# Kernel optimization log

Measured on AMD Instinct MI355X. Metric: run time of the kernel, lower is better.

## Reference

```python
import jax, jax.numpy as jnp
import numpy as np

ALPHA = 0.5  # mixing weight between dot-product and wedge-norm terms


def setup_inputs() -> dict:
    key = jax.random.key(0)
    kq, kk, kv = jax.random.split(key, 3)
    B, L, H, E = 2, 2048, 8, 32
    queries = jax.random.normal(kq, (B, L, H, E), dtype=jnp.float32)
    keys = jax.random.normal(kk, (B, L, H, E), dtype=jnp.float32)
    values = jax.random.normal(kv, (B, L, H, E), dtype=jnp.float32)
    return {"queries": queries, "keys": keys, "values": values}


def reference(queries, keys, values):
    # queries: [B,L,H,E], keys: [B,S,H,E], values: [B,S,H,D]
    E = queries.shape[-1]
    scale = 1.0 / jnp.sqrt(jnp.asarray(E, dtype=queries.dtype))
    # dot product scores: [B,H,L,S]
    dot = jnp.einsum('blhe,bshe->bhls', queries, keys)
    # squared norms -> broadcastable [B,H,L,1] and [B,H,1,S]
    qn2 = jnp.sum(queries ** 2, axis=-1).transpose(0, 2, 1)[..., :, None]
    kn2 = jnp.sum(keys ** 2, axis=-1).transpose(0, 2, 1)[..., None, :]
    # wedge (Clifford) squared norm, clamped at 0
    wedge = jax.nn.relu(qn2 * kn2 - dot ** 2)
    scores = (ALPHA * dot - (1.0 - ALPHA) * wedge) * scale
    attn = jax.nn.softmax(scores, axis=-1)  # [B,H,L,S]
    # out: [B,L,H,D]
    out = jnp.einsum('bhls,bshd->blhd', attn, values)
    return out
```

## Files before the change

### kernel.cpp

```cpp
#include <hip/hip_runtime.h>
#include <hip/hip_bf16.h>
#include <math.h>


#define NB 2
#define NL 2048
#define NS 2048
#define NH 8
#define NBH 16
#define STRIPS 4
#define NT 8
#define CSC 0.12751742f
#define DEFER_THR 24.0f

#define WS_KN2_OFF 0u
#define WS_KHKL_OFF 131072u
#define WS_VT_OFF (131072u + 4194304u)
#define WS_PACC_OFF (131072u + 4194304u + 2097152u)
#define WS_PML_OFF (WS_PACC_OFF + 16777216u)
#define WS_NEED (WS_PML_OFF + 1048576u)

typedef float f32x4 __attribute__((ext_vector_type(4)));
typedef float f32x2 __attribute__((ext_vector_type(2)));
typedef short s16x8 __attribute__((ext_vector_type(8)));
typedef unsigned short u16;

__device__ inline unsigned pk2(float a, float b) {
    __hip_bfloat162 t = __float22bfloat162_rn(make_float2(a, b));
    union { __hip_bfloat162 h; unsigned u; } cv;
    cv.h = t;
    return cv.u;
}
template <int CTRL>
__device__ inline float dpp_add(float x) {
    return x + __int_as_float(__builtin_amdgcn_mov_dpp(__float_as_int(x), CTRL, 0xF, 0xF, false));
}
__device__ inline void dma16(const void* gp, void* lp) {
    __builtin_amdgcn_global_load_lds(
        (__attribute__((address_space(1))) void*)(void*)gp,
        (__attribute__((address_space(3))) void*)lp, 16, 0, 0);
}
__device__ inline void pl32(unsigned& a, unsigned& b) {
    asm("v_permlane32_swap_b32 %0, %1" : "+v"(a), "+v"(b));
}
__device__ inline void pl16(unsigned& a, unsigned& b) {
    asm("v_permlane16_swap_b32 %0, %1" : "+v"(a), "+v"(b));
}
__device__ inline int swzK(int row) { return (row ^ (row >> 2)) & 3; }
__device__ inline int swzV(int row) { return (row + (row >> 3)) & 7; }

__global__ __launch_bounds__(256) void ga_pre(const float* __restrict__ K,
                                              const float* __restrict__ V,
                                              float* __restrict__ kn2w,
                                              u16* __restrict__ khkl,
                                              u16* __restrict__ vtw) {
    __shared__ float Vf[64][36];
    const int T = threadIdx.x;
    const int bh = blockIdx.x >> 5, stile = blockIdx.x & 31;
    const int b = bh >> 3, h = bh & 7;
    const int s0 = stile * 64;
    const int sk = T >> 2, kc = T & 3;

    const float* kp = K + ((size_t)((b * NS + s0 + sk) * NH + h)) * 32 + kc * 8;
    float4 f0 = *(const float4*)kp, f1 = *(const float4*)(kp + 4);
    float kx[8] = {f0.x, f0.y, f0.z, f0.w, f1.x, f1.y, f1.z, f1.w};
    unsigned hh[4], ll[4];
    float kn2p = 0.f;
#pragma unroll
    for (int i = 0; i < 4; i++) {
        float x0 = kx[2 * i], x1 = kx[2 * i + 1];
        kn2p = fmaf(x0, x0, kn2p);
        kn2p = fmaf(x1, x1, kn2p);
        unsigned h01 = pk2(x0, x1);
        hh[i] = h01;
        float h0 = __uint_as_float(h01 << 16);
        float h1 = __uint_as_float(h01 & 0xffff0000u);
        ll[i] = pk2(x0 - h0, x1 - h1);
    }
    u16* kd = khkl + ((size_t)(bh * NS + s0 + sk)) * 64;
    const int swk = sk & 7;
    *(uint4*)(kd + ((kc ^ swk) * 8)) = make_uint4(hh[0], hh[1], hh[2], hh[3]);
    *(uint4*)(kd + (((4 + kc) ^ swk) * 8)) = make_uint4(ll[0], ll[1], ll[2], ll[3]);
    kn2p = dpp_add<0xB1>(kn2p);
    kn2p = dpp_add<0x4E>(kn2p);
    if (kc == 0) kn2w[bh * NS + s0 + sk] = kn2p;

    const float* vp = V + ((size_t)((b * NS + s0 + sk) * NH + h)) * 32 + kc * 8;
    float4 g0 = *(const float4*)vp, g1 = *(const float4*)(vp + 4);
    const int chv = kc ^ ((sk >> 3) & 3);
    *(float4*)&Vf[sk][chv * 8] = g0;
    *(float4*)&Vf[sk][chv * 8 + 4] = g1;
    __syncthreads();
    const int dr = T >> 3, c = T & 7;
    float vv[8];
#pragma unroll
    for (int i = 0; i < 8; i++)
        vv[i] = Vf[c * 8 + i][(((dr >> 3) ^ (c & 3)) << 3) + (dr & 7)];
    const int phys = c ^ (dr & 7);
    *(uint4*)(vtw + ((size_t)(bh * 32 + dr)) * NS + s0 + phys * 8) =
        make_uint4(pk2(vv[0], vv[1]), pk2(vv[2], vv[3]), pk2(vv[4], vv[5]), pk2(vv[6], vv[7]));
}

__global__ __launch_bounds__(256, 3) void ga_dma(
    const float* __restrict__ Q, const float* __restrict__ kn2w,
    const u16* __restrict__ khkl, const u16* __restrict__ vtw,
    float* __restrict__ pacc, float* __restrict__ pml) {
    __shared__ u16 sK[2][64][64];
    __shared__ u16 sV[2][32][64];

    const int T = threadIdx.x;
    const int lane = T & 63, wave = T >> 6;
    const int g = lane >> 4, lc = lane & 15, g8 = g * 8;
    const int blk = blockIdx.x;
    const int qt = blk & 15, strip = (blk >> 4) & 3, bh = blk >> 6;
    const int b = bh >> 3, h = bh & 7;
    const int qwa = qt * 128 + wave * 16;
    const int qwb = qwa + 64;
    const int kb0 = strip * 512;

    s16x8 qha, qla, qhb, qlb;
    float qn2a, qn2b;
    {
        const float* qrow = Q + ((size_t)((b * NL + qwa + lc) * NH + h)) * 32 + g8;
        float4 qa = *(const float4*)qrow, qb = *(const float4*)(qrow + 4);
        float q8[8] = {qa.x, qa.y, qa.z, qa.w, qb.x, qb.y, qb.z, qb.w};
        union { unsigned u4[4]; s16x8 v; } qh_, ql_;
        float qn2 = 0.f;
#pragma unroll
        for (int i = 0; i < 4; i++) {
            float x0 = q8[2 * i], x1 = q8[2 * i + 1];
            qn2 = fmaf(x0, x0, qn2);
            qn2 = fmaf(x1, x1, qn2);
            unsigned h01 = pk2(x0, x1);
            qh_.u4[i] = h01;
            float h0 = __uint_as_float(h01 << 16);
            float h1 = __uint_as_float(h01 & 0xffff0000u);
            ql_.u4[i] = pk2(x0 - h0, x1 - h1);
        }
        qha = qh_.v; qla = ql_.v;
        qn2 += __shfl_xor(qn2, 16);
        qn2 += __shfl_xor(qn2, 32);
        qn2a = qn2;
    }
    {
        const float* qrow = Q + ((size_t)((b * NL + qwb + lc) * NH + h)) * 32 + g8;
        float4 qa = *(const float4*)qrow, qb = *(const float4*)(qrow + 4);
        float q8[8] = {qa.x, qa.y, qa.z, qa.w, qb.x, qb.y, qb.z, qb.w};
        union { unsigned u4[4]; s16x8 v; } qh_, ql_;
        float qn2 = 0.f;
#pragma unroll
        for (int i = 0; i < 4; i++) {
            float x0 = q8[2 * i], x1 = q8[2 * i + 1];
            qn2 = fmaf(x0, x0, qn2);
            qn2 = fmaf(x1, x1, qn2);
            unsigned h01 = pk2(x0, x1);
            qh_.u4[i] = h01;
            float h0 = __uint_as_float(h01 << 16);
            float h1 = __uint_as_float(h01 & 0xffff0000u);
            ql_.u4[i] = pk2(x0 - h0, x1 - h1);
        }
        qhb = qh_.v; qlb = ql_.v;
        qn2 += __shfl_xor(qn2, 16);
        qn2 += __shfl_xor(qn2, 32);
        qn2b = qn2;
    }

    const char* ksrc = (const char*)khkl +
        ((size_t)(bh * NS + kb0 + 16 * wave)) * 128 + lane * 16;
    const char* vsrc = (const char*)vtw +
        ((size_t)(bh * 32 + 8 * wave + (lane >> 3))) * (NS * 2) +
        (size_t)(kb0 + (lane & 7) * 8) * 2;
    const float* kn2b = kn2w + (size_t)bh * NS + kb0 + 4 * g;

    dma16(ksrc, &sK[0][16 * wave][0]);
    dma16(ksrc + 1024, &sK[0][16 * wave + 8][0]);
    dma16(vsrc, &sV[0][8 * wave][0]);
    __syncthreads();

    s16x8 ones;
#pragma unroll
    for (int i = 0; i < 8; i++) ones[i] = (short)0x3F80;

    f32x4 acc0a = {0.f, 0.f, 0.f, 0.f}, acc1a = {0.f, 0.f, 0.f, 0.f};
    f32x4 acc0b = {0.f, 0.f, 0.f, 0.f}, acc1b = {0.f, 0.f, 0.f, 0.f};
    f32x4 lacca = {0.f, 0.f, 0.f, 0.f}, laccb = {0.f, 0.f, 0.f, 0.f};
    float ma = -1e30f, mb = -1e30f;
    const f32x4 z = {0.f, 0.f, 0.f, 0.f};
    const int sw = lc & 7;

#pragma unroll 1
    for (int t = 0; t < NT; ++t) {
        const int cur = t & 1;
        if (t + 1 < NT) {
            const char* k2 = ksrc + (size_t)(t + 1) * 8192;
            const char* v2 = vsrc + (size_t)(t + 1) * 128;
            dma16(k2, &sK[cur ^ 1][16 * wave][0]);
            dma16(k2 + 1024, &sK[cur ^ 1][16 * wave + 8][0]);
            dma16(v2, &sV[cur ^ 1][8 * wave][0]);
        }

        f32x4 da[4], db[4], kn2m[4];
#pragma unroll
        for (int st = 0; st < 4; st++) {
            kn2m[st] = *(const f32x4*)(kn2b + t * 64 + 16 * st);
            s16x8 kh = *(s16x8*)&sK[cur][16 * st + lc][(g ^ sw) * 8];
            s16x8 klo = *(s16x8*)&sK[cur][16 * st + lc][((4 + g) ^ sw) * 8];
            f32x4 dd = __builtin_amdgcn_mfma_f32_16x16x32_bf16(klo, qha, z, 0, 0, 0);
            dd = __builtin_amdgcn_mfma_f32_16x16x32_bf16(kh, qla, dd, 0, 0, 0);
            da[st] = __builtin_amdgcn_mfma_f32_16x16x32_bf16(kh, qha, dd, 0, 0, 0);
            f32x4 de = __builtin_amdgcn_mfma_f32_16x16x32_bf16(klo, qhb, z, 0, 0, 0);
            de = __builtin_amdgcn_mfma_f32_16x16x32_bf16(kh, qlb, de, 0, 0, 0);
            db[st] = __builtin_amdgcn_mfma_f32_16x16x32_bf16(kh, qhb, de, 0, 0, 0);
        }
        s16x8 va0 = *(s16x8*)&sV[cur][lc][(g ^ sw) * 8];
        s16x8 va1 = *(s16x8*)&sV[cur][lc][((4 + g) ^ sw) * 8];
        s16x8 va2 = *(s16x8*)&sV[cur][lc + 16][(g ^ sw) * 8];
        s16x8 va3 = *(s16x8*)&sV[cur][lc + 16][((4 + g) ^ sw) * 8];

        float sca[4][4], scb[4][4];
        {
            const f32x2 qa2 = {qn2a, qn2a}, qb2 = {qn2b, qn2b};
#pragma unroll
            for (int st = 0; st < 4; st++) {
                f32x2 kk0 = {kn2m[st][0], kn2m[st][1]}, kk1 = {kn2m[st][2], kn2m[st][3]};
                f32x2 dd0 = {da[st][0], da[st][1]}, dd1 = {da[st][2], da[st][3]};
                f32x2 e0 = dd0 - qa2 * kk0;
                f32x2 e1 = dd1 - qa2 * kk1;
                f32x2 t0 = dd0 * dd0 + e0;
                f32x2 t1 = dd1 * dd1 + e1;
                sca[st][0] = fminf(da[st][0], t0[0]);
                sca[st][1] = fminf(da[st][1], t0[1]);
                sca[st][2] = fminf(da[st][2], t1[0]);
                sca[st][3] = fminf(da[st][3], t1[1]);
                f32x2 ee0 = {db[st][0], db[st][1]}, ee1 = {db[st][2], db[st][3]};
                f32x2 f0 = ee0 - qb2 * kk0;
                f32x2 f1 = ee1 - qb2 * kk1;
                f32x2 u0 = ee0 * ee0 + f0;
                f32x2 u1 = ee1 * ee1 + f1;
                scb[st][0] = fminf(db[st][0], u0[0]);
                scb[st][1] = fminf(db[st][1], u0[1]);
                scb[st][2] = fminf(db[st][2], u1[0]);
                scb[st][3] = fminf(db[st][3], u1[1]);
            }
        }

        float a0 = fmaxf(fmaxf(sca[0][0], sca[0][1]), fmaxf(sca[0][2], sca[0][3]));
        float a1 = fmaxf(fmaxf(sca[1][0], sca[1][1]), fmaxf(sca[1][2], sca[1][3]));
        float a2 = fmaxf(fmaxf(sca[2][0], sca[2][1]), fmaxf(sca[2][2], sca[2][3]));
        float a3 = fmaxf(fmaxf(sca[3][0], sca[3][1]), fmaxf(sca[3][2], sca[3][3]));
        float tma = fmaxf(fmaxf(a0, a1), fmaxf(a2, a3));
        float b0 = fmaxf(fmaxf(scb[0][0], scb[0][1]), fmaxf(scb[0][2], scb[0][3]));
        float b1 = fmaxf(fmaxf(scb[1][0], scb[1][1]), fmaxf(scb[1][2], scb[1][3]));
        float b2 = fmaxf(fmaxf(scb[2][0], scb[2][1]), fmaxf(scb[2][2], scb[2][3]));
        float b3 = fmaxf(fmaxf(scb[3][0], scb[3][1]), fmaxf(scb[3][2], scb[3][3]));
        float tmb = fmaxf(fmaxf(b0, b1), fmaxf(b2, b3));
        if (!__all((tma <= ma + DEFER_THR) && (tmb <= mb + DEFER_THR))) {
            tma = fmaxf(tma, __shfl_xor(tma, 16));
            tma = fmaxf(tma, __shfl_xor(tma, 32));
            tmb = fmaxf(tmb, __shfl_xor(tmb, 16));
            tmb = fmaxf(tmb, __shfl_xor(tmb, 32));
            const float nma = fmaxf(ma, tma), nmb = fmaxf(mb, tmb);
            const float ala = __builtin_amdgcn_exp2f((ma - nma) * CSC);
            const float alb = __builtin_amdgcn_exp2f((mb - nmb) * CSC);
            ma = nma; mb = nmb;
            acc0a *= ala; acc1a *= ala; lacca *= ala;
            acc0b *= alb; acc1b *= alb; laccb *= alb;
        }
        const float negmaC = -ma * CSC, negmbC = -mb * CSC;
        const f32x2 cscv = {CSC, CSC};
        const f32x2 nmav = {negmaC, negmaC}, nmbv = {negmbC, negmbC};
        float pa[4][4], pb[4][4];
#pragma unroll
        for (int st = 0; st < 4; st++) {
            f32x2 s0 = {sca[st][0], sca[st][1]}, s1 = {sca[st][2], sca[st][3]};
            f32x2 e0 = s0 * cscv + nmav;
            f32x2 e1 = s1 * cscv + nmav;
            pa[st][0] = __builtin_amdgcn_exp2f(e0[0]);
            pa[st][1] = __builtin_amdgcn_exp2f(e0[1]);
            pa[st][2] = __builtin_amdgcn_exp2f(e1[0]);
            pa[st][3] = __builtin_amdgcn_exp2f(e1[1]);
            f32x2 u0 = {scb[st][0], scb[st][1]}, u1 = {scb[st][2], scb[st][3]};
            f32x2 f0 = u0 * cscv + nmbv;
            f32x2 f1 = u1 * cscv + nmbv;
            pb[st][0] = __builtin_amdgcn_exp2f(f0[0]);
            pb[st][1] = __builtin_amdgcn_exp2f(f0[1]);
            pb[st][2] = __builtin_amdgcn_exp2f(f1[0]);
            pb[st][3] = __builtin_amdgcn_exp2f(f1[1]);
        }

        {
            unsigned w00 = pk2(pa[0][0], pa[0][1]), w01 = pk2(pa[0][2], pa[0][3]);
            unsigned w10 = pk2(pa[1][0], pa[1][1]), w11 = pk2(pa[1][2], pa[1][3]);
            unsigned w20 = pk2(pa[2][0], pa[2][1]), w21 = pk2(pa[2][2], pa[2][3]);
            unsigned w30 = pk2(pa[3][0], pa[3][1]), w31 = pk2(pa[3][2], pa[3][3]);
            pl32(w00, w10); pl32(w01, w11);
            pl16(w00, w10); pl16(w01, w11);
            pl32(w20, w30); pl32(w21, w31);
            pl16(w20, w30); pl16(w21, w31);
            union { uint4 u; s16x8 v; } P0, P1;
            P0.u = make_uint4(w00, w01, w10, w11);
            P1.u = make_uint4(w20, w21, w30, w31);
            acc0a = __builtin_amdgcn_mfma_f32_16x16x32_bf16(va0, P0.v, acc0a, 0, 0, 0);
            acc0a = __builtin_amdgcn_mfma_f32_16x16x32_bf16(va1, P1.v, acc0a, 0, 0, 0);
            acc1a = __builtin_amdgcn_mfma_f32_16x16x32_bf16(va2, P0.v, acc1a, 0, 0, 0);
            acc1a = __builtin_amdgcn_mfma_f32_16x16x32_bf16(va3, P1.v, acc1a, 0, 0, 0);
            lacca = __builtin_amdgcn_mfma_f32_16x16x32_bf16(ones, P0.v, lacca, 0, 0, 0);
            lacca = __builtin_amdgcn_mfma_f32_16x16x32_bf16(ones, P1.v, lacca, 0, 0, 0);
        }
        {
            unsigned w00 = pk2(pb[0][0], pb[0][1]), w01 = pk2(pb[0][2], pb[0][3]);
            unsigned w10 = pk2(pb[1][0], pb[1][1]), w11 = pk2(pb[1][2], pb[1][3]);
            unsigned w20 = pk2(pb[2][0], pb[2][1]), w21 = pk2(pb[2][2], pb[2][3]);
            unsigned w30 = pk2(pb[3][0], pb[3][1]), w31 = pk2(pb[3][2], pb[3][3]);
            pl32(w00, w10); pl32(w01, w11);
            pl16(w00, w10); pl16(w01, w11);
            pl32(w20, w30); pl32(w21, w31);
            pl16(w20, w30); pl16(w21, w31);
            union { uint4 u; s16x8 v; } P0, P1;
            P0.u = make_uint4(w00, w01, w10, w11);
            P1.u = make_uint4(w20, w21, w30, w31);
            acc0b = __builtin_amdgcn_mfma_f32_16x16x32_bf16(va0, P0.v, acc0b, 0, 0, 0);
            acc0b = __builtin_amdgcn_mfma_f32_16x16x32_bf16(va1, P1.v, acc0b, 0, 0, 0);
            acc1b = __builtin_amdgcn_mfma_f32_16x16x32_bf16(va2, P0.v, acc1b, 0, 0, 0);
            acc1b = __builtin_amdgcn_mfma_f32_16x16x32_bf16(va3, P1.v, acc1b, 0, 0, 0);
            laccb = __builtin_amdgcn_mfma_f32_16x16x32_bf16(ones, P0.v, laccb, 0, 0, 0);
            laccb = __builtin_amdgcn_mfma_f32_16x16x32_bf16(ones, P1.v, laccb, 0, 0, 0);
        }

        __syncthreads();
    }

    float* paa = pacc + (((size_t)bh * STRIPS + strip) * NL + (qwa + lc)) * 32;
    *(f32x4*)(paa + 4 * g) = acc0a;
    *(f32x4*)(paa + 16 + 4 * g) = acc1a;
    float* pab = pacc + (((size_t)bh * STRIPS + strip) * NL + (qwb + lc)) * 32;
    *(f32x4*)(pab + 4 * g) = acc0b;
    *(f32x4*)(pab + 16 + 4 * g) = acc1b;
    if (g == 0) {
        *(float2*)(pml + (((size_t)bh * STRIPS + strip) * NL + (qwa + lc)) * 2) =
            make_float2(ma, lacca[0]);
        *(float2*)(pml + (((size_t)bh * STRIPS + strip) * NL + (qwb + lc)) * 2) =
            make_float2(mb, laccb[0]);
    }
}

__global__ __launch_bounds__(256) void ga_combine(const float* __restrict__ pacc,
                                                  const float* __restrict__ pml,
                                                  float* __restrict__ O) {
    const int tid = blockIdx.x * 256 + threadIdx.x;
    const int dq = tid & 7, q = (tid >> 3) & 2047, bh = tid >> 14;
    const int b = bh >> 3, h = bh & 7;
    float m[4], l[4];
#pragma unroll
    for (int s = 0; s < 4; s++) {
        float2 t = *(const float2*)(pml + (((size_t)bh * STRIPS + s) * NL + q) * 2);
        m[s] = t.x;
        l[s] = t.y;
    }
    float mf = fmaxf(fmaxf(m[0], m[1]), fmaxf(m[2], m[3]));
    float w[4], L = 0.f;
#pragma unroll
    for (int s = 0; s < 4; s++) {
        w[s] = __builtin_amdgcn_exp2f((m[s] - mf) * CSC);
        L = fmaf(l[s], w[s], L);
    }
    const float inv = 1.f / L;
    float4 o = make_float4(0.f, 0.f, 0.f, 0.f);
#pragma unroll
    for (int s = 0; s < 4; s++) {
        const float* pa = pacc + (((size_t)bh * STRIPS + s) * NL + q) * 32 + dq * 4;
        float4 a = *(const float4*)pa;
        o.x = fmaf(a.x, w[s], o.x);
        o.y = fmaf(a.y, w[s], o.y);
        o.z = fmaf(a.z, w[s], o.z);
        o.w = fmaf(a.w, w[s], o.w);
    }
    o.x *= inv; o.y *= inv; o.z *= inv; o.w *= inv;
    *(float4*)(O + (((size_t)(b * NL + q)) * NH + h) * 32 + dq * 4) = o;
}

__global__ __launch_bounds__(512, 4) void ga_fallback(
    const float* __restrict__ Q, const float* __restrict__ K,
    const float* __restrict__ V, float* __restrict__ O) {
    __shared__ union {
        struct {
            u16 Kh[2][64][32];
            u16 Kl[2][64][32];
            u16 Vt[2][32][64];
            float kn2[2][64];
        } s;
        struct { float acc[8][32][17]; float m[8][16]; float l[8][16]; } c;
    } u;
    __shared__ u16 sP[8][16][64];

    const int T = threadIdx.x;
    const int lane = T & 63, wave = T >> 6;
    const int g = lane >> 4, lc = lane & 15, g8 = g * 8;
    const int half = wave >> 2;
    const int qt = blockIdx.x & 31;
    const int bh = blockIdx.x >> 5;
    const int b = bh >> 3, h = bh & 7;
    const int qw = qt * 64 + (wave & 3) * 16;

    const float* qrow = Q + ((size_t)((b * NL + qw + lc) * NH + h)) * 32 + g8;
    float4 qa = *(const float4*)qrow, qb = *(const float4*)(qrow + 4);
    float q8[8] = {qa.x, qa.y, qa.z, qa.w, qb.x, qb.y, qb.z, qb.w};
    union { unsigned u4[4]; s16x8 v; } qh_, ql_;
    float qn2 = 0.f;
#pragma unroll
    for (int i = 0; i < 4; i++) {
        float x0 = q8[2 * i], x1 = q8[2 * i + 1];
        qn2 = fmaf(x0, x0, qn2);
        qn2 = fmaf(x1, x1, qn2);
        unsigned h01 = pk2(x0, x1);
        qh_.u4[i] = h01;
        float h0 = __uint_as_float(h01 << 16);
        float h1 = __uint_as_float(h01 & 0xffff0000u);
        ql_.u4[i] = pk2(x0 - h0, x1 - h1);
    }
    const s16x8 qh = qh_.v, ql = ql_.v;
    qn2 += __shfl_xor(qn2, 16);
    qn2 += __shfl_xor(qn2, 32);

    const int Tl = T & 255;
    const int sk = Tl >> 2, kc = Tl & 3;
    const int dv = Tl & 31, vc = Tl >> 5;
    const float* kbase = K + ((size_t)(b * NS * NH) + h) * 32;
    const float* vbase = V + ((size_t)(b * NS * NH) + h) * 32;
    const int kphys = (kc ^ swzK(sk)) * 8;
    const int vphys = (vc ^ swzV(dv)) * 8;

    int s0 = half * 1024;
    float4 ka = *(const float4*)(kbase + (size_t)(s0 + sk) * 256 + kc * 8);
    float4 kb = *(const float4*)(kbase + (size_t)(s0 + sk) * 256 + kc * 8 + 4);
    float vr[8];
#pragma unroll
    for (int i = 0; i < 8; i++) vr[i] = vbase[(size_t)(s0 + 8 * vc + i) * 256 + dv];

    f32x4 acc0 = {0.f, 0.f, 0.f, 0.f}, acc1 = {0.f, 0.f, 0.f, 0.f};
    float m = -INFINITY, l = 0.f;

    for (int t = 0; t < 16; ++t) {
        {
            float kx[8] = {ka.x, ka.y, ka.z, ka.w, kb.x, kb.y, kb.z, kb.w};
            unsigned hh[4], ll[4];
            float kn2p = 0.f;
#pragma unroll
            for (int i = 0; i < 4; i++) {
                float x0 = kx[2 * i], x1 = kx[2 * i + 1];
                kn2p = fmaf(x0, x0, kn2p);
                kn2p = fmaf(x1, x1, kn2p);
                unsigned h01 = pk2(x0, x1);
                hh[i] = h01;
                float h0 = __uint_as_float(h01 << 16);
                float h1 = __uint_as_float(h01 & 0xffff0000u);
                ll[i] = pk2(x0 - h0, x1 - h1);
            }
            *(uint4*)&u.s.Kh[half][sk][kphys] = make_uint4(hh[0], hh[1], hh[2], hh[3]);
            *(uint4*)&u.s.Kl[half][sk][kphys] = make_uint4(ll[0], ll[1], ll[2], ll[3]);
            kn2p = dpp_add<0xB1>(kn2p);
            kn2p = dpp_add<0x4E>(kn2p);
            if (kc == 0) u.s.kn2[half][sk] = kn2p;
            *(uint4*)&u.s.Vt[half][dv][vphys] =
                make_uint4(pk2(vr[0], vr[1]), pk2(vr[2], vr[3]),
                           pk2(vr[4], vr[5]), pk2(vr[6], vr[7]));
        }
        const int tn = (t + 1 < 16) ? t + 1 : t;
        const int sn = half * 1024 + tn * 64;
        ka = *(const float4*)(kbase + (size_t)(sn + sk) * 256 + kc * 8);
        kb = *(const float4*)(kbase + (size_t)(sn + sk) * 256 + kc * 8 + 4);
#pragma unroll
        for (int i = 0; i < 8; i++) vr[i] = vbase[(size_t)(sn + 8 * vc + i) * 256 + dv];

        __syncthreads();

        f32x4 d[4], kn2v[4];
        const f32x4 z = {0.f, 0.f, 0.f, 0.f};
        const int skr = swzK(lc);
#pragma unroll
        for (int st = 0; st < 4; st++) {
            kn2v[st] = *(f32x4*)&u.s.kn2[half][16 * st + 4 * g];
            s16x8 kh = *(s16x8*)&u.s.Kh[half][16 * st + lc][(g ^ skr) * 8];
            s16x8 kl = *(s16x8*)&u.s.Kl[half][16 * st + lc][(g ^ skr) * 8];
            f32x4 dd = __builtin_amdgcn_mfma_f32_16x16x32_bf16(kl, qh, z, 0, 0, 0);
            dd = __builtin_amdgcn_mfma_f32_16x16x32_bf16(kh, ql, dd, 0, 0, 0);
            dd = __builtin_amdgcn_mfma_f32_16x16x32_bf16(kh, qh, dd, 0, 0, 0);
            d[st] = dd;
        }

        float sc[4][4];
#pragma unroll
        for (int st = 0; st < 4; st++)
#pragma unroll
            for (int r = 0; r < 4; r++) {
                float dd = d[st][r];
                float w = fmaxf(fmaf(-dd, dd, qn2 * kn2v[st][r]), 0.f);
                sc[st][r] = (dd - w) * CSC;
            }

        float x0 = fmaxf(fmaxf(sc[0][0], sc[0][1]), fmaxf(sc[0][2], sc[0][3]));
        float x1 = fmaxf(fmaxf(sc[1][0], sc[1][1]), fmaxf(sc[1][2], sc[1][3]));
        float x2 = fmaxf(fmaxf(sc[2][0], sc[2][1]), fmaxf(sc[2][2], sc[2][3]));
        float x3 = fmaxf(fmaxf(sc[3][0], sc[3][1]), fmaxf(sc[3][2], sc[3][3]));
        float tm = fmaxf(fmaxf(x0, x1), fmaxf(x2, x3));
        tm = fmaxf(tm, __shfl_xor(tm, 16));
        tm = fmaxf(tm, __shfl_xor(tm, 32));
        const float nm = fmaxf(m, tm);
        const float al = __builtin_amdgcn_exp2f(m - nm);
        m = nm;
        float p[4][4], ls = 0.f;
#pragma unroll
        for (int st = 0; st < 4; st++)
#pragma unroll
            for (int r = 0; r < 4; r++) {
                p[st][r] = __builtin_amdgcn_exp2f(sc[st][r] - nm);
                ls += p[st][r];
            }
        l = fmaf(l, al, ls);
        acc0 *= al;
        acc1 *= al;

#pragma unroll
        for (int st = 0; st < 4; st++) {
            const int off = ((2 * st + (g >> 1)) ^ (lc & 7)) * 8 + (g & 1) * 4;
            *(uint2*)&sP[wave][lc][off] =
                make_uint2(pk2(p[st][0], p[st][1]), pk2(p[st][2], p[st][3]));
        }
        __builtin_amdgcn_s_waitcnt(0xC07F);

        const int svl = swzV(lc), svh = swzV(lc + 16), spl = lc & 7;
        s16x8 va00 = *(s16x8*)&u.s.Vt[half][lc][(g ^ svl) * 8];
        s16x8 va01 = *(s16x8*)&u.s.Vt[half][lc][((4 + g) ^ svl) * 8];
        s16x8 va10 = *(s16x8*)&u.s.Vt[half][lc + 16][(g ^ svh) * 8];
        s16x8 va11 = *(s16x8*)&u.s.Vt[half][lc + 16][((4 + g) ^ svh) * 8];
        s16x8 pb0 = *(s16x8*)&sP[wave][lc][(g ^ spl) * 8];
        s16x8 pb1 = *(s16x8*)&sP[wave][lc][((4 + g) ^ spl) * 8];
        acc0 = __builtin_amdgcn_mfma_f32_16x16x32_bf16(va00, pb0, acc0, 0, 0, 0);
        acc0 = __builtin_amdgcn_mfma_f32_16x16x32_bf16(va01, pb1, acc0, 0, 0, 0);
        acc1 = __builtin_amdgcn_mfma_f32_16x16x32_bf16(va10, pb0, acc1, 0, 0, 0);
        acc1 = __builtin_amdgcn_mfma_f32_16x16x32_bf16(va11, pb1, acc1, 0, 0, 0);

        __syncthreads();
    }

    l += __shfl_xor(l, 16);
    l += __shfl_xor(l, 32);
#pragma unroll
    for (int r = 0; r < 4; r++) {
        u.c.acc[wave][4 * g + r][lc] = acc0[r];
        u.c.acc[wave][16 + 4 * g + r][lc] = acc1[r];
    }
    if (lane < 16) {
        u.c.m[wave][lc] = m;
        u.c.l[wave][lc] = l;
    }
    __syncthreads();

    const int q = T >> 3, dq = (T & 7) * 4, qr = q & 15;
    const int w0 = q >> 4, w1 = w0 + 4;
    float m0 = u.c.m[w0][qr], m1 = u.c.m[w1][qr];
    float l0 = u.c.l[w0][qr], l1 = u.c.l[w1][qr];
    float mf = fmaxf(m0, m1);
    float e0 = __builtin_amdgcn_exp2f(m0 - mf);
    float e1 = __builtin_amdgcn_exp2f(m1 - mf);
    float inv = 1.f / fmaf(l1, e1, l0 * e0);
    e0 *= inv;
    e1 *= inv;
    float4 o;
    o.x = u.c.acc[w0][dq + 0][qr] * e0 + u.c.acc[w1][dq + 0][qr] * e1;
    o.y = u.c.acc[w0][dq + 1][qr] * e0 + u.c.acc[w1][dq + 1][qr] * e1;
    o.z = u.c.acc[w0][dq + 2][qr] * e0 + u.c.acc[w1][dq + 2][qr] * e1;
    o.w = u.c.acc[w0][dq + 3][qr] * e0 + u.c.acc[w1][dq + 3][qr] * e1;
    *(float4*)(O + ((size_t)((b * NL + qt * 64 + q) * NH + h)) * 32 + dq) = o;
}

extern "C" void kernel_launch(void* const* d_in, const int* in_sizes, int n_in,
                              void* d_out, int out_size, void* d_ws, size_t ws_size,
                              hipStream_t stream) {
    const float* Q = (const float*)d_in[0];
    const float* K = (const float*)d_in[1];
    const float* V = (const float*)d_in[2];
    float* O = (float*)d_out;

    if (ws_size >= (size_t)WS_NEED) {
        float* kn2w = (float*)((char*)d_ws + WS_KN2_OFF);
        u16* khkl = (u16*)((char*)d_ws + WS_KHKL_OFF);
        u16* vtw = (u16*)((char*)d_ws + WS_VT_OFF);
        float* pacc = (float*)((char*)d_ws + WS_PACC_OFF);
        float* pml = (float*)((char*)d_ws + WS_PML_OFF);
        ga_pre<<<NBH * 32, 256, 0, stream>>>(K, V, kn2w, khkl, vtw);
        ga_dma<<<NBH * 16 * STRIPS, 256, 0, stream>>>(Q, kn2w, khkl, vtw, pacc, pml);
        ga_combine<<<(NBH * NL * 8) / 256, 256, 0, stream>>>(pacc, pml, O);
    } else {
        ga_fallback<<<NBH * 32, 512, 0, stream>>>(Q, K, V, O);
    }
}
```

Baseline: 105.0 us.

## Give each wave private K/V staging buffers and drop block-wide barriers

The attention kernel now lets each wave stream its own copy of every K/V tile into a private double-buffered shared-memory region. It uses explicit vmcnt/lgkmcnt waits instead of a block-wide __syncthreads per iteration. Tiles shrink from 64 to 32 keys (twice as many iterations), and the V transpose layout drops its XOR swizzle so each wave reads V rows directly. This removes inter-wave barrier stalls, but each block now loads every K/V tile four times, which raises L2 and DMA traffic and doubles LDS usage per block.

```diff
diff --git a/kernel.cpp b/kernel.cpp
--- a/kernel.cpp
+++ b/kernel.cpp
@@ -9,7 +9,7 @@
 #define NH 8
 #define NBH 16
 #define STRIPS 4
-#define NT 8
+#define NT 16
 #define CSC 0.12751742f
 #define DEFER_THR 24.0f
 
@@ -96,17 +96,16 @@
 #pragma unroll
     for (int i = 0; i < 8; i++)
         vv[i] = Vf[c * 8 + i][(((dr >> 3) ^ (c & 3)) << 3) + (dr & 7)];
-    const int phys = c ^ (dr & 7);
-    *(uint4*)(vtw + ((size_t)(bh * 32 + dr)) * NS + s0 + phys * 8) =
+    *(uint4*)(vtw + ((size_t)(bh * 32 + dr)) * NS + s0 + c * 8) =
         make_uint4(pk2(vv[0], vv[1]), pk2(vv[2], vv[3]), pk2(vv[4], vv[5]), pk2(vv[6], vv[7]));
 }
 
-__global__ __launch_bounds__(256, 3) void ga_dma(
+__global__ __launch_bounds__(256, 3) void ga_wave(
     const float* __restrict__ Q, const float* __restrict__ kn2w,
     const u16* __restrict__ khkl, const u16* __restrict__ vtw,
     float* __restrict__ pacc, float* __restrict__ pml) {
-    __shared__ u16 sK[2][64][64];
-    __shared__ u16 sV[2][32][64];
+    __shared__ u16 sK[4][2][32][64];
+    __shared__ u16 sV[4][2][32][32];
 
     const int T = threadIdx.x;
     const int lane = T & 63, wave = T >> 6;
@@ -165,17 +164,22 @@
         qn2b = qn2;
     }
 
-    const char* ksrc = (const char*)khkl +
-        ((size_t)(bh * NS + kb0 + 16 * wave)) * 128 + lane * 16;
+    const char* ksrc = (const char*)khkl + (size_t)(bh * NS + kb0) * 128 + lane * 16;
     const char* vsrc = (const char*)vtw +
-        ((size_t)(bh * 32 + 8 * wave + (lane >> 3))) * (NS * 2) +
-        (size_t)(kb0 + (lane & 7) * 8) * 2;
+        ((size_t)(bh * 32 + (lane >> 2)) * NS + kb0 + (lane & 3) * 8) * 2;
     const float* kn2b = kn2w + (size_t)bh * NS + kb0 + 4 * g;
 
-    dma16(ksrc, &sK[0][16 * wave][0]);
-    dma16(ksrc + 1024, &sK[0][16 * wave + 8][0]);
-    dma16(vsrc, &sV[0][8 * wave][0]);
-    __syncthreads();
+    u16(*mK)[32][64] = sK[wave];
+    u16(*mV)[32][32] = sV[wave];
+
+    {
+        dma16(ksrc, &mK[0][0][0]);
+        dma16(ksrc + 1024, &mK[0][8][0]);
+        dma16(ksrc + 2048, &mK[0][16][0]);
+        dma16(ksrc + 3072, &mK[0][24][0]);
+        dma16(vsrc, &mV[0][0][0]);
+        dma16(vsrc + 16 * NS * 2, &mV[0][16][0]);
+    }
 
     s16x8 ones;
 #pragma unroll
@@ -190,70 +194,82 @@
 
 #pragma unroll 1
     for (int t = 0; t < NT; ++t) {
-        const int cur = t & 1;
+        asm volatile("s_waitcnt lgkmcnt(0)" ::: "memory");
+        f32x4 kn20 = *(const f32x4*)(kn2b + t * 32);
+        f32x4 kn21 = *(const f32x4*)(kn2b + t * 32 + 16);
+        __builtin_amdgcn_sched_barrier(0);
         if (t + 1 < NT) {
-            const char* k2 = ksrc + (size_t)(t + 1) * 8192;
-            const char* v2 = vsrc + (size_t)(t + 1) * 128;
-            dma16(k2, &sK[cur ^ 1][16 * wave][0]);
-            dma16(k2 + 1024, &sK[cur ^ 1][16 * wave + 8][0]);
-            dma16(v2, &sV[cur ^ 1][8 * wave][0]);
-        }
-
-        f32x4 da[4], db[4], kn2m[4];
-#pragma unroll
-        for (int st = 0; st < 4; st++) {
-            kn2m[st] = *(const f32x4*)(kn2b + t * 64 + 16 * st);
-            s16x8 kh = *(s16x8*)&sK[cur][16 * st + lc][(g ^ sw) * 8];
-            s16x8 klo = *(s16x8*)&sK[cur][16 * st + lc][((4 + g) ^ sw) * 8];
-            f32x4 dd = __builtin_amdgcn_mfma_f32_16x16x32_bf16(klo, qha, z, 0, 0, 0);
-            dd = __builtin_amdgcn_mfma_f32_16x16x32_bf16(kh, qla, dd, 0, 0, 0);
-            da[st] = __builtin_amdgcn_mfma_f32_16x16x32_bf16(kh, qha, dd, 0, 0, 0);
-            f32x4 de = __builtin_amdgcn_mfma_f32_16x16x32_bf16(klo, qhb, z, 0, 0, 0);
-            de = __builtin_amdgcn_mfma_f32_16x16x32_bf16(kh, qlb, de, 0, 0, 0);
-            db[st] = __builtin_amdgcn_mfma_f32_16x16x32_bf16(kh, qhb, de, 0, 0, 0);
-        }
-        s16x8 va0 = *(s16x8*)&sV[cur][lc][(g ^ sw) * 8];
-        s16x8 va1 = *(s16x8*)&sV[cur][lc][((4 + g) ^ sw) * 8];
-        s16x8 va2 = *(s16x8*)&sV[cur][lc + 16][(g ^ sw) * 8];
-        s16x8 va3 = *(s16x8*)&sV[cur][lc + 16][((4 + g) ^ sw) * 8];
-
-        float sca[4][4], scb[4][4];
+            const char* k2 = ksrc + (size_t)(t + 1) * 4096;
+            const char* v2 = vsrc + (size_t)(t + 1) * 64;
+            const int nb = (t + 1) & 1;
+            dma16(k2, &mK[nb][0][0]);
+            dma16(k2 + 1024, &mK[nb][8][0]);
+            dma16(k2 + 2048, &mK[nb][16][0]);
+            dma16(k2 + 3072, &mK[nb][24][0]);
+            dma16(v2, &mV[nb][0][0]);
+            dma16(v2 + 16 * NS * 2, &mV[nb][16][0]);
+            asm volatile("s_waitcnt vmcnt(6)" ::: "memory");
+        } else {
+            asm volatile("s_waitcnt vmcnt(0)" ::: "memory");
+        }
+        __builtin_amdgcn_sched_barrier(0);
+
+        const int buf = t & 1;
+        s16x8 kh0 = *(s16x8*)&mK[buf][lc][(g ^ sw) * 8];
+        s16x8 kl0 = *(s16x8*)&mK[buf][lc][((4 + g) ^ sw) * 8];
+        s16x8 kh1 = *(s16x8*)&mK[buf][16 + lc][(g ^ sw) * 8];
+        s16x8 kl1 = *(s16x8*)&mK[buf][16 + lc][((4 + g) ^ sw) * 8];
+        f32x4 da0, da1, db0, db1;
+        {
+            f32x4 dd = __builtin_amdgcn_mfma_f32_16x16x32_bf16(kl0, qha, z, 0, 0, 0);
+            dd = __builtin_amdgcn_mfma_f32_16x16x32_bf16(kh0, qla, dd, 0, 0, 0);
+            da0 = __builtin_amdgcn_mfma_f32_16x16x32_bf16(kh0, qha, dd, 0, 0, 0);
+            dd = __builtin_amdgcn_mfma_f32_16x16x32_bf16(kl1, qha, z, 0, 0, 0);
+            dd = __builtin_amdgcn_mfma_f32_16x16x32_bf16(kh1, qla, dd, 0, 0, 0);
+            da1 = __builtin_amdgcn_mfma_f32_16x16x32_bf16(kh1, qha, dd, 0, 0, 0);
+            dd = __builtin_amdgcn_mfma_f32_16x16x32_bf16(kl0, qhb, z, 0, 0, 0);
+            dd = __builtin_amdgcn_mfma_f32_16x16x32_bf16(kh0, qlb, dd, 0, 0, 0);
+            db0 = __builtin_amdgcn_mfma_f32_16x16x32_bf16(kh0, qhb, dd, 0, 0, 0);
+            dd = __builtin_amdgcn_mfma_f32_16x16x32_bf16(kl1, qhb, z, 0, 0, 0);
+            dd = __builtin_amdgcn_mfma_f32_16x16x32_bf16(kh1, qlb, dd, 0, 0, 0);
+            db1 = __builtin_amdgcn_mfma_f32_16x16x32_bf16(kh1, qhb, dd, 0, 0, 0);
+        }
+        s16x8 vlo = *(s16x8*)&mV[buf][lc][g8];
+        s16x8 vhi = *(s16x8*)&mV[buf][16 + lc][g8];
+
+        float sca[2][4], scb[2][4];
         {
             const f32x2 qa2 = {qn2a, qn2a}, qb2 = {qn2b, qn2b};
-#pragma unroll
-            for (int st = 0; st < 4; st++) {
+            f32x4 kn2m[2] = {kn20, kn21};
+            f32x4 dam[2] = {da0, da1}, dbm[2] = {db0, db1};
+#pragma unroll
+            for (int st = 0; st < 2; st++) {
                 f32x2 kk0 = {kn2m[st][0], kn2m[st][1]}, kk1 = {kn2m[st][2], kn2m[st][3]};
-                f32x2 dd0 = {da[st][0], da[st][1]}, dd1 = {da[st][2], da[st][3]};
+                f32x2 dd0 = {dam[st][0], dam[st][1]}, dd1 = {dam[st][2], dam[st][3]};
                 f32x2 e0 = dd0 - qa2 * kk0;
                 f32x2 e1 = dd1 - qa2 * kk1;
                 f32x2 t0 = dd0 * dd0 + e0;
                 f32x2 t1 = dd1 * dd1 + e1;
-                sca[st][0] = fminf(da[st][0], t0[0]);
-                sca[st][1] = fminf(da[st][1], t0[1]);
-                sca[st][2] = fminf(da[st][2], t1[0]);
-                sca[st][3] = fminf(da[st][3], t1[1]);
-                f32x2 ee0 = {db[st][0], db[st][1]}, ee1 = {db[st][2], db[st][3]};
+                sca[st][0] = fminf(dam[st][0], t0[0]);
+                sca[st][1] = fminf(dam[st][1], t0[1]);
+                sca[st][2] = fminf(dam[st][2], t1[0]);
+                sca[st][3] = fminf(dam[st][3], t1[1]);
+                f32x2 ee0 = {dbm[st][0], dbm[st][1]}, ee1 = {dbm[st][2], dbm[st][3]};
                 f32x2 f0 = ee0 - qb2 * kk0;
                 f32x2 f1 = ee1 - qb2 * kk1;
                 f32x2 u0 = ee0 * ee0 + f0;
                 f32x2 u1 = ee1 * ee1 + f1;
-                scb[st][0] = fminf(db[st][0], u0[0]);
-                scb[st][1] = fminf(db[st][1], u0[1]);
-                scb[st][2] = fminf(db[st][2], u1[0]);
-                scb[st][3] = fminf(db[st][3], u1[1]);
+                scb[st][0] = fminf(dbm[st][0], u0[0]);
+                scb[st][1] = fminf(dbm[st][1], u0[1]);
+                scb[st][2] = fminf(dbm[st][2], u1[0]);
+                scb[st][3] = fminf(dbm[st][3], u1[1]);
             }
         }
 
-        float a0 = fmaxf(fmaxf(sca[0][0], sca[0][1]), fmaxf(sca[0][2], sca[0][3]));
-        float a1 = fmaxf(fmaxf(sca[1][0], sca[1][1]), fmaxf(sca[1][2], sca[1][3]));
-        float a2 = fmaxf(fmaxf(sca[2][0], sca[2][1]), fmaxf(sca[2][2], sca[2][3]));
-        float a3 = fmaxf(fmaxf(sca[3][0], sca[3][1]), fmaxf(sca[3][2], sca[3][3]));
-        float tma = fmaxf(fmaxf(a0, a1), fmaxf(a2, a3));
-        float b0 = fmaxf(fmaxf(scb[0][0], scb[0][1]), fmaxf(scb[0][2], scb[0][3]));
-        float b1 = fmaxf(fmaxf(scb[1][0], scb[1][1]), fmaxf(scb[1][2], scb[1][3]));
-        float b2 = fmaxf(fmaxf(scb[2][0], scb[2][1]), fmaxf(scb[2][2], scb[2][3]));
-        float b3 = fmaxf(fmaxf(scb[3][0], scb[3][1]), fmaxf(scb[3][2], scb[3][3]));
-        float tmb = fmaxf(fmaxf(b0, b1), fmaxf(b2, b3));
+        float tma = fmaxf(fmaxf(fmaxf(sca[0][0], sca[0][1]), fmaxf(sca[0][2], sca[0][3])),
+                          fmaxf(fmaxf(sca[1][0], sca[1][1]), fmaxf(sca[1][2], sca[1][3])));
+        float tmb = fmaxf(fmaxf(fmaxf(scb[0][0], scb[0][1]), fmaxf(scb[0][2], scb[0][3])),
+                          fmaxf(fmaxf(scb[1][0], scb[1][1]), fmaxf(scb[1][2], scb[1][3])));
         if (!__all((tma <= ma + DEFER_THR) && (tmb <= mb + DEFER_THR))) {
             tma = fmaxf(tma, __shfl_xor(tma, 16));
             tma = fmaxf(tma, __shfl_xor(tma, 32));
@@ -269,9 +285,9 @@
         const float negmaC = -ma * CSC, negmbC = -mb * CSC;
         const f32x2 cscv = {CSC, CSC};
         const f32x2 nmav = {negmaC, negmaC}, nmbv = {negmbC, negmbC};
-        float pa[4][4], pb[4][4];
-#pragma unroll
-        for (int st = 0; st < 4; st++) {
+        float pa[2][4], pb[2][4];
+#pragma unroll
+        for (int st = 0; st < 2; st++) {
             f32x2 s0 = {sca[st][0], sca[st][1]}, s1 = {sca[st][2], sca[st][3]};
             f32x2 e0 = s0 * cscv + nmav;
             f32x2 e1 = s1 * cscv + nmav;
@@ -291,43 +307,25 @@
         {
             unsigned w00 = pk2(pa[0][0], pa[0][1]), w01 = pk2(pa[0][2], pa[0][3]);
             unsigned w10 = pk2(pa[1][0], pa[1][1]), w11 = pk2(pa[1][2], pa[1][3]);
-            unsigned w20 = pk2(pa[2][0], pa[2][1]), w21 = pk2(pa[2][2], pa[2][3]);
-            unsigned w30 = pk2(pa[3][0], pa[3][1]), w31 = pk2(pa[3][2], pa[3][3]);
             pl32(w00, w10); pl32(w01, w11);
             pl16(w00, w10); pl16(w01, w11);
-            pl32(w20, w30); pl32(w21, w31);
-            pl16(w20, w30); pl16(w21, w31);
-            union { uint4 u; s16x8 v; } P0, P1;
-            P0.u = make_uint4(w00, w01, w10, w11);
-            P1.u = make_uint4(w20, w21, w30, w31);
-            acc0a = __builtin_amdgcn_mfma_f32_16x16x32_bf16(va0, P0.v, acc0a, 0, 0, 0);
-            acc0a = __builtin_amdgcn_mfma_f32_16x16x32_bf16(va1, P1.v, acc0a, 0, 0, 0);
-            acc1a = __builtin_amdgcn_mfma_f32_16x16x32_bf16(va2, P0.v, acc1a, 0, 0, 0);
-            acc1a = __builtin_amdgcn_mfma_f32_16x16x32_bf16(va3, P1.v, acc1a, 0, 0, 0);
-            lacca = __builtin_amdgcn_mfma_f32_16x16x32_bf16(ones, P0.v, lacca, 0, 0, 0);
-            lacca = __builtin_amdgcn_mfma_f32_16x16x32_bf16(ones, P1.v, lacca, 0, 0, 0);
+            union { uint4 u; s16x8 v; } P;
+            P.u = make_uint4(w00, w01, w10, w11);
+            acc0a = __builtin_amdgcn_mfma_f32_16x16x32_bf16(vlo, P.v, acc0a, 0, 0, 0);
+            acc1a = __builtin_amdgcn_mfma_f32_16x16x32_bf16(vhi, P.v, acc1a, 0, 0, 0);
+            lacca = __builtin_amdgcn_mfma_f32_16x16x32_bf16(ones, P.v, lacca, 0, 0, 0);
         }
         {
             unsigned w00 = pk2(pb[0][0], pb[0][1]), w01 = pk2(pb[0][2], pb[0][3]);
             unsigned w10 = pk2(pb[1][0], pb[1][1]), w11 = pk2(pb[1][2], pb[1][3]);
-            unsigned w20 = pk2(pb[2][0], pb[2][1]), w21 = pk2(pb[2][2], pb[2][3]);
-            unsigned w30 = pk2(pb[3][0], pb[3][1]), w31 = pk2(pb[3][2], pb[3][3]);
             pl32(w00, w10); pl32(w01, w11);
             pl16(w00, w10); pl16(w01, w11);
-            pl32(w20, w30); pl32(w21, w31);
-            pl16(w20, w30); pl16(w21, w31);
-            union { uint4 u; s16x8 v; } P0, P1;
-            P0.u = make_uint4(w00, w01, w10, w11);
-            P1.u = make_uint4(w20, w21, w30, w31);
-            acc0b = __builtin_amdgcn_mfma_f32_16x16x32_bf16(va0, P0.v, acc0b, 0, 0, 0);
-            acc0b = __builtin_amdgcn_mfma_f32_16x16x32_bf16(va1, P1.v, acc0b, 0, 0, 0);
-            acc1b = __builtin_amdgcn_mfma_f32_16x16x32_bf16(va2, P0.v, acc1b, 0, 0, 0);
-            acc1b = __builtin_amdgcn_mfma_f32_16x16x32_bf16(va3, P1.v, acc1b, 0, 0, 0);
-            laccb = __builtin_amdgcn_mfma_f32_16x16x32_bf16(ones, P0.v, laccb, 0, 0, 0);
-            laccb = __builtin_amdgcn_mfma_f32_16x16x32_bf16(ones, P1.v, laccb, 0, 0, 0);
-        }
-
-        __syncthreads();
+            union { uint4 u; s16x8 v; } P;
+            P.u = make_uint4(w00, w01, w10, w11);
+            acc0b = __builtin_amdgcn_mfma_f32_16x16x32_bf16(vlo, P.v, acc0b, 0, 0, 0);
+            acc1b = __builtin_amdgcn_mfma_f32_16x16x32_bf16(vhi, P.v, acc1b, 0, 0, 0);
+            laccb = __builtin_amdgcn_mfma_f32_16x16x32_bf16(ones, P.v, laccb, 0, 0, 0);
+        }
     }
 
     float* paa = pacc + (((size_t)bh * STRIPS + strip) * NL + (qwa + lc)) * 32;
@@ -589,7 +587,7 @@
         float* pacc = (float*)((char*)d_ws + WS_PACC_OFF);
         float* pml = (float*)((char*)d_ws + WS_PML_OFF);
         ga_pre<<<NBH * 32, 256, 0, stream>>>(K, V, kn2w, khkl, vtw);
-        ga_dma<<<NBH * 16 * STRIPS, 256, 0, stream>>>(Q, kn2w, khkl, vtw, pacc, pml);
+        ga_wave<<<NBH * 16 * STRIPS, 256, 0, stream>>>(Q, kn2w, khkl, vtw, pacc, pml);
         ga_combine<<<(NBH * NL * 8) / 256, 256, 0, stream>>>(pacc, pml, O);
     } else {
         ga_fallback<<<NBH * 32, 512, 0, stream>>>(Q, K, V, O);
```

Result: no change. 106.8 us (+1.7%).
